# Optimization experiments

Measured on AMD Instinct MI355X. Metric: run time of the kernel, lower is better.

## Reference

```python
import jax, jax.numpy as jnp
import numpy as np

B, T, H, V = 4, 512, 2048, 32000
BETA = 0.1          # KL coefficient vs reference model
EPS_LOW = 0.2       # PPO clip lower
EPS_HIGH = 0.2      # PPO clip upper
TEMP = 1.0          # logit temperature


def _per_token_logps(h, w, ids):
    # h: [B,T,H], w: [V,H], ids: [B,T] -> log p(token_id) per position
    logits = jnp.einsum('bth,vh->btv', h, w) / TEMP          # [B,T,V]
    logps = jax.nn.log_softmax(logits.astype(jnp.float32), axis=-1)
    return jnp.take_along_axis(logps, ids[..., None], axis=-1)[..., 0]  # [B,T]


def setup_inputs() -> dict:
    key = jax.random.key(0)
    k = jax.random.split(key, 6)
    x = jax.random.normal(k[0], (B, T, H), jnp.float32)
    ref_input = jax.random.normal(k[1], (B, T, H), jnp.float32)
    lin_weight = jax.random.normal(k[2], (V, H), jnp.float32) * (H ** -0.5)
    ref_weight = jax.random.normal(k[3], (V, H), jnp.float32) * (H ** -0.5)
    selected_token_ids = jax.random.randint(k[4], (B, T), 0, V)
    attention_mask = jnp.ones((B, T), jnp.int32)
    advantages = jax.random.normal(k[5], (B,), jnp.float32)
    return {
        'x': x,
        'lin_weight': lin_weight,
        'ref_input': ref_input,
        'ref_weight': ref_weight,
        'advantages': advantages,
        'selected_token_ids': selected_token_ids,
        'attention_mask': attention_mask,
    }


def reference(x, lin_weight, ref_input, ref_weight, advantages,
              selected_token_ids, attention_mask):
    # policy per-token log-probs (fused linear + log-softmax + gather)
    logps = _per_token_logps(x, lin_weight, selected_token_ids)            # [B,T]
    # reference model path runs under no_grad in the original
    ref_logps = jax.lax.stop_gradient(
        _per_token_logps(ref_input, ref_weight, selected_token_ids))      # [B,T]
    # old_per_token_logps=None -> detached current logps (ratio==1 in fwd)
    old_logps = jax.lax.stop_gradient(logps)

    coef1 = jnp.exp(logps - old_logps)
    coef2 = jnp.clip(coef1, 1.0 - EPS_LOW, 1.0 + EPS_HIGH)
    adv = advantages[:, None]                                             # [B,1]
    per_token_loss = -jnp.minimum(coef1 * adv, coef2 * adv)

    # KL(ref || policy) surrogate: exp(d) - d - 1 with d = ref - cur
    d = ref_logps - logps
    kl = jnp.exp(d) - d - 1.0
    per_token_loss = per_token_loss + BETA * kl

    mask = attention_mask.astype(jnp.float32)
    # loss_type='bnpo': global masked token mean
    loss = jnp.sum(per_token_loss * mask) / jnp.maximum(jnp.sum(mask), 1.0)
    return loss
```

## Files before the change

### kernel.cpp

```cpp
#include <hip/hip_runtime.h>
#include <hip/hip_bf16.h>

#define B_ 4
#define T_ 512
#define H_ 2048
#define V_ 32000
#define M_ (B_ * T_)
#define BETA_ 0.1f

#define BM 128
#define BN 128
#define BK 32
#define NTILES (V_ / BN)
#define NP (NTILES * 2)
#define NPAD 512
#define GRID_LIN 4096

typedef __attribute__((ext_vector_type(8))) short short8;
typedef __attribute__((ext_vector_type(4))) float f32x4;

__device__ __forceinline__ void async_copy16(const void* g, void* l) {
  __builtin_amdgcn_global_load_lds(
      (const __attribute__((address_space(1))) void*)g,
      (__attribute__((address_space(3))) void*)l, 16, 0, 0);
}

__device__ __forceinline__ unsigned short f2bf(float f) {
  unsigned int u = __float_as_uint(f);
  u += 0x7fffu + ((u >> 16) & 1u);
  return (unsigned short)(u >> 16);
}

__global__ void cvt_bf16_kernel(const float* __restrict__ in,
                                unsigned short* __restrict__ out, int n4) {
  int i = blockIdx.x * blockDim.x + threadIdx.x;
  if (i < n4) {
    float4 v = ((const float4*)in)[i];
    ushort4 o;
    o.x = f2bf(v.x); o.y = f2bf(v.y); o.z = f2bf(v.z); o.w = f2bf(v.w);
    ((ushort4*)out)[i] = o;
  }
}

__global__ void sel_kernel(const float* __restrict__ x, const float* __restrict__ w,
                           const float* __restrict__ rx, const float* __restrict__ rw,
                           const int* __restrict__ ids, float* __restrict__ sel) {
  int gw = (blockIdx.x * 256 + threadIdx.x) >> 6;
  int l = threadIdx.x & 63;
  int md = gw >> 11;
  int m = gw & (M_ - 1);
  const float* xr = (md ? rx : x) + (size_t)m * H_;
  const float* wr = (md ? rw : w) + (size_t)ids[m] * H_;
  float s = 0.0f;
#pragma unroll
  for (int it = 0; it < H_ / 256; ++it) {
    int k = it * 256 + l * 4;
    float4 a = *(const float4*)(xr + k);
    float4 b = *(const float4*)(wr + k);
    s += a.x * b.x + a.y * b.y + a.z * b.z + a.w * b.w;
  }
#pragma unroll
  for (int off = 32; off; off >>= 1) s += __shfl_xor(s, off, 64);
  if (l == 0) sel[md * M_ + m] = s;
}

__global__ __launch_bounds__(256) void gemm_lse_kernel(
    const unsigned short* __restrict__ A,
    const unsigned short* __restrict__ Bw,
    float* __restrict__ pmax,
    float* __restrict__ psum) {
  const int linear = blockIdx.x;
  const int nt = (linear & 7) + 8 * (linear >> 7);
  if (nt >= NTILES) return;
  const int mb = (linear >> 3) & 15;

  __shared__ char smem[(BM + BN) * BK * 2];
  char* As = smem;
  char* Bs = smem + BM * BK * 2;

  const int tid = threadIdx.x;
  const int w = tid >> 6, l = tid & 63;
  const int quad = l >> 4, lr = l & 15;
  const int m0 = mb * BM, n0 = nt * BN;
  const int wm = (w >> 1) * 64, wn = (w & 1) * 64;

  const int s0 = tid, s1 = tid + 256;
  const unsigned short* gA0 = A + (size_t)(m0 + (s0 & 127)) * H_ + (s0 >> 7) * 8;
  const unsigned short* gA1 = A + (size_t)(m0 + (s1 & 127)) * H_ + (s1 >> 7) * 8;
  const unsigned short* gB0 = Bw + (size_t)(n0 + (s0 & 127)) * H_ + (s0 >> 7) * 8;
  const unsigned short* gB1 = Bw + (size_t)(n0 + (s1 & 127)) * H_ + (s1 >> 7) * 8;
  char* lA0 = As + s0 * 16; char* lA1 = As + s1 * 16;
  char* lB0 = Bs + s0 * 16; char* lB1 = Bs + s1 * 16;

  f32x4 acc[4][4] = {};

  const char* aRd[4]; const char* bRd[4];
#pragma unroll
  for (int i = 0; i < 4; ++i) {
    aRd[i] = As + (quad * 128 + wm + i * 16 + lr) * 16;
    bRd[i] = Bs + (quad * 128 + wn + i * 16 + lr) * 16;
  }

  for (int kt = 0; kt < H_ / BK; ++kt) {
    async_copy16(gA0, lA0); async_copy16(gA1, lA1);
    async_copy16(gB0, lB0); async_copy16(gB1, lB1);
    gA0 += BK; gA1 += BK; gB0 += BK; gB1 += BK;
    __syncthreads();
    short8 af[4], bf[4];
#pragma unroll
    for (int i = 0; i < 4; ++i) af[i] = *(const short8*)aRd[i];
#pragma unroll
    for (int j = 0; j < 4; ++j) bf[j] = *(const short8*)bRd[j];
#pragma unroll
    for (int i = 0; i < 4; ++i)
#pragma unroll
      for (int j = 0; j < 4; ++j)
        acc[i][j] = __builtin_amdgcn_mfma_f32_16x16x32_bf16(af[i], bf[j], acc[i][j], 0, 0, 0);
    __syncthreads();
  }

  const int p_idx = nt * 2 + (w & 1);
#pragma unroll
  for (int i = 0; i < 4; ++i) {
#pragma unroll
    for (int r = 0; r < 4; ++r) {
      float vmax = fmaxf(fmaxf(acc[i][0][r], acc[i][1][r]),
                         fmaxf(acc[i][2][r], acc[i][3][r]));
#pragma unroll
      for (int off = 8; off; off >>= 1) vmax = fmaxf(vmax, __shfl_xor(vmax, off, 64));
      float s = __expf(acc[i][0][r] - vmax) + __expf(acc[i][1][r] - vmax) +
                __expf(acc[i][2][r] - vmax) + __expf(acc[i][3][r] - vmax);
#pragma unroll
      for (int off = 8; off; off >>= 1) s += __shfl_xor(s, off, 64);
      if (lr == 0) {
        int mg = m0 + wm + i * 16 + quad * 4 + r;
        pmax[(size_t)mg * NPAD + p_idx] = vmax;
        psum[(size_t)mg * NPAD + p_idx] = s;
      }
    }
  }
}

__global__ void lse_merge_kernel(
    const float* __restrict__ pmaxP, const float* __restrict__ psumP,
    const float* __restrict__ pmaxR, const float* __restrict__ psumR,
    const float* __restrict__ sel, float* __restrict__ lp) {
  int gw = (blockIdx.x * 256 + threadIdx.x) >> 6;
  int l = threadIdx.x & 63;
  int md = gw >> 11, m = gw & (M_ - 1);
  const float* pm = (md ? pmaxR : pmaxP) + (size_t)m * NPAD;
  const float* ps = (md ? psumR : psumP) + (size_t)m * NPAD;
  float mx = -3.0e38f, s = 0.0f;
  for (int p = l; p < NP; p += 64) {
    float a = pm[p], b = ps[p];
    float nm = fmaxf(mx, a);
    s = s * __expf(mx - nm) + b * __expf(a - nm);
    mx = nm;
  }
#pragma unroll
  for (int off = 32; off; off >>= 1) {
    float omx = __shfl_xor(mx, off, 64);
    float os  = __shfl_xor(s, off, 64);
    float nm = fmaxf(mx, omx);
    s = s * __expf(mx - nm) + os * __expf(omx - nm);
    mx = nm;
  }
  if (l == 0) lp[md * M_ + m] = sel[md * M_ + m] - (mx + __logf(s));
}

__global__ void loss_kernel(const float* __restrict__ lp,
                            const float* __restrict__ adv,
                            const int* __restrict__ mask,
                            float* __restrict__ out) {
  __shared__ float sp[16], sm[16];
  int t = threadIdx.x;
  float pt = 0.0f, mk = 0.0f;
  for (int m = t; m < M_; m += 1024) {
    float d = lp[M_ + m] - lp[m];
    float kl = __expf(d) - d - 1.0f;
    float mkm = (float)mask[m];
    pt += (-adv[m >> 9] + BETA_ * kl) * mkm;
    mk += mkm;
  }
#pragma unroll
  for (int off = 32; off; off >>= 1) {
    pt += __shfl_xor(pt, off, 64);
    mk += __shfl_xor(mk, off, 64);
  }
  int wv = t >> 6, l = t & 63;
  if (l == 0) { sp[wv] = pt; sm[wv] = mk; }
  __syncthreads();
  if (t == 0) {
    float a = 0.0f, b = 0.0f;
#pragma unroll
    for (int i = 0; i < 16; ++i) { a += sp[i]; b += sm[i]; }
    out[0] = a / fmaxf(b, 1.0f);
  }
}

extern "C" void kernel_launch(void* const* d_in, const int* in_sizes, int n_in,
                              void* d_out, int out_size, void* d_ws, size_t ws_size,
                              hipStream_t stream) {
  const float* x    = (const float*)d_in[0];
  const float* lw   = (const float*)d_in[1];
  const float* rx   = (const float*)d_in[2];
  const float* rw   = (const float*)d_in[3];
  const float* adv  = (const float*)d_in[4];
  const int*   ids  = (const int*)d_in[5];
  const int*   mask = (const int*)d_in[6];
  float* out = (float*)d_out;

  char* ws = (char*)d_ws;
  unsigned short* Wb = (unsigned short*)ws;
  unsigned short* xb = (unsigned short*)(ws + (size_t)V_ * H_ * 2);
  char* p0 = ws + (size_t)V_ * H_ * 2 + (size_t)M_ * H_ * 2;
  const size_t PSZ = (size_t)M_ * NPAD * 4;
  float* pmaxP = (float*)(p0);
  float* psumP = (float*)(p0 + 1 * PSZ);
  float* pmaxR = (float*)(p0 + 2 * PSZ);
  float* psumR = (float*)(p0 + 3 * PSZ);
  float* sel   = (float*)(p0 + 4 * PSZ);
  float* lp    = (float*)(p0 + 4 * PSZ + 2 * M_ * 4);

  const int n4x = M_ * H_ / 4, n4w = V_ * H_ / 4;

  cvt_bf16_kernel<<<(n4x + 255) / 256, 256, 0, stream>>>(x, xb, n4x);
  cvt_bf16_kernel<<<(n4w + 255) / 256, 256, 0, stream>>>(lw, Wb, n4w);
  sel_kernel<<<(2 * M_) / 4, 256, 0, stream>>>(x, lw, rx, rw, ids, sel);
  gemm_lse_kernel<<<GRID_LIN, 256, 0, stream>>>(xb, Wb, pmaxP, psumP);
  cvt_bf16_kernel<<<(n4x + 255) / 256, 256, 0, stream>>>(rx, xb, n4x);
  cvt_bf16_kernel<<<(n4w + 255) / 256, 256, 0, stream>>>(rw, Wb, n4w);
  gemm_lse_kernel<<<GRID_LIN, 256, 0, stream>>>(xb, Wb, pmaxR, psumR);

  lse_merge_kernel<<<(2 * M_) / 4, 256, 0, stream>>>(pmaxP, psumP, pmaxR, psumR,
                                                     sel, lp);
  loss_kernel<<<1, 1024, 0, stream>>>(lp, adv, mask, out);
}
```

Before: 1.656 ms.

## Enlarge GEMM tiles to 256x256x64 with double-buffered LDS pipeline

The fused GEMM+LSE kernel moves from 128x128x32 tiles with 4 waves to 256x256x64 tiles with 8 waves. Each wave now computes a 128x64 sub-tile, and the LDS buffers are double-buffered so that global-to-LDS async loads of the next K slice overlap the MFMAs on the current one, with one barrier per iteration. s_setprio is raised around the MFMA bursts. The aim is more data reuse per loaded byte and fewer barrier stalls. The costs are 128 KB of dynamic LDS, higher register pressure from 32 accumulators per wave, and fewer blocks (125x8 tiles) to fill the CUs.

After: 1.689 ms. Within noise of the previous version (+2.0%).

```diff
diff --git a/kernel.cpp b/kernel.cpp
--- a/kernel.cpp
+++ b/kernel.cpp
@@ -8,13 +8,18 @@
 #define M_ (B_ * T_)
 #define BETA_ 0.1f
 
-#define BM 128
-#define BN 128
-#define BK 32
+#define BM 256
+#define BN 256
+#define BK 64
+#define NKT (H_ / BK)
 #define NTILES (V_ / BN)
-#define NP (NTILES * 2)
+#define NP (NTILES * 4)
 #define NPAD 512
-#define GRID_LIN 4096
+#define GRID_GEMM 1024
+
+#define ABYTES (BM * BK * 2)
+#define BUFBYTES (2 * ABYTES)
+#define LDS_TOTAL (2 * BUFBYTES)
 
 typedef __attribute__((ext_vector_type(8))) short short8;
 typedef __attribute__((ext_vector_type(4))) float f32x4;
@@ -64,64 +69,84 @@
   if (l == 0) sel[md * M_ + m] = s;
 }
 
-__global__ __launch_bounds__(256) void gemm_lse_kernel(
+__global__ __launch_bounds__(512, 2) void gemm_lse_kernel(
     const unsigned short* __restrict__ A,
     const unsigned short* __restrict__ Bw,
     float* __restrict__ pmax,
     float* __restrict__ psum) {
   const int linear = blockIdx.x;
-  const int nt = (linear & 7) + 8 * (linear >> 7);
+  const int c = linear & 7, g = linear >> 3;
+  const int nt = (g >> 3) * 8 + c;
   if (nt >= NTILES) return;
-  const int mb = (linear >> 3) & 15;
-
-  __shared__ char smem[(BM + BN) * BK * 2];
-  char* As = smem;
-  char* Bs = smem + BM * BK * 2;
+  const int mb = g & 7;
+
+  extern __shared__ char smem[];
 
   const int tid = threadIdx.x;
   const int w = tid >> 6, l = tid & 63;
   const int quad = l >> 4, lr = l & 15;
+  const int wr = w >> 2, wc = w & 3;
   const int m0 = mb * BM, n0 = nt * BN;
-  const int wm = (w >> 1) * 64, wn = (w & 1) * 64;
-
-  const int s0 = tid, s1 = tid + 256;
-  const unsigned short* gA0 = A + (size_t)(m0 + (s0 & 127)) * H_ + (s0 >> 7) * 8;
-  const unsigned short* gA1 = A + (size_t)(m0 + (s1 & 127)) * H_ + (s1 >> 7) * 8;
-  const unsigned short* gB0 = Bw + (size_t)(n0 + (s0 & 127)) * H_ + (s0 >> 7) * 8;
-  const unsigned short* gB1 = Bw + (size_t)(n0 + (s1 & 127)) * H_ + (s1 >> 7) * 8;
-  char* lA0 = As + s0 * 16; char* lA1 = As + s1 * 16;
-  char* lB0 = Bs + s0 * 16; char* lB1 = Bs + s1 * 16;
-
-  f32x4 acc[4][4] = {};
-
-  const char* aRd[4]; const char* bRd[4];
-#pragma unroll
-  for (int i = 0; i < 4; ++i) {
-    aRd[i] = As + (quad * 128 + wm + i * 16 + lr) * 16;
-    bRd[i] = Bs + (quad * 128 + wn + i * 16 + lr) * 16;
-  }
-
-  for (int kt = 0; kt < H_ / BK; ++kt) {
-    async_copy16(gA0, lA0); async_copy16(gA1, lA1);
-    async_copy16(gB0, lB0); async_copy16(gB1, lB1);
-    gA0 += BK; gA1 += BK; gB0 += BK; gB1 += BK;
+
+  const int srow = tid & 255, shi = tid >> 8;
+  const unsigned short* gA = A + (size_t)(m0 + srow) * H_ + shi * 8;
+  const unsigned short* gB = Bw + (size_t)(n0 + srow) * H_ + shi * 8;
+  const int ldsoff = (shi * 256 + srow) * 16;
+
+  f32x4 acc[8][4] = {};
+
+  const int abOff = quad * 4096 + (wr * 128 + lr) * 16;
+  const int bbOff = ABYTES + quad * 4096 + (wc * 64 + lr) * 16;
+
+  auto stage = [&](int p, int kt) {
+    const unsigned short* a = gA + kt * BK;
+    const unsigned short* b = gB + kt * BK;
+    char* la = smem + p * BUFBYTES + ldsoff;
+    char* lb = la + ABYTES;
+#pragma unroll
+    for (int j = 0; j < 4; ++j) {
+      async_copy16(a + j * 16, la + j * 8192);
+      async_copy16(b + j * 16, lb + j * 8192);
+    }
+  };
+
+  auto compute = [&](int p) {
+    const char* ab = smem + p * BUFBYTES + abOff;
+    const char* bb = smem + p * BUFBYTES + bbOff;
+#pragma unroll
+    for (int kk = 0; kk < 2; ++kk) {
+      short8 af[8], bf[4];
+#pragma unroll
+      for (int i = 0; i < 8; ++i)
+        af[i] = *(const short8*)(ab + kk * 16384 + i * 256);
+#pragma unroll
+      for (int j = 0; j < 4; ++j)
+        bf[j] = *(const short8*)(bb + kk * 16384 + j * 256);
+      __builtin_amdgcn_s_setprio(1);
+#pragma unroll
+      for (int i = 0; i < 8; ++i)
+#pragma unroll
+        for (int j = 0; j < 4; ++j)
+          acc[i][j] = __builtin_amdgcn_mfma_f32_16x16x32_bf16(
+              af[i], bf[j], acc[i][j], 0, 0, 0);
+      __builtin_amdgcn_s_setprio(0);
+    }
+  };
+
+  stage(0, 0);
+  __syncthreads();
+  int p = 0;
+  for (int kt = 1; kt < NKT; ++kt) {
+    stage(p ^ 1, kt);
+    compute(p);
     __syncthreads();
-    short8 af[4], bf[4];
-#pragma unroll
-    for (int i = 0; i < 4; ++i) af[i] = *(const short8*)aRd[i];
-#pragma unroll
-    for (int j = 0; j < 4; ++j) bf[j] = *(const short8*)bRd[j];
-#pragma unroll
-    for (int i = 0; i < 4; ++i)
-#pragma unroll
-      for (int j = 0; j < 4; ++j)
-        acc[i][j] = __builtin_amdgcn_mfma_f32_16x16x32_bf16(af[i], bf[j], acc[i][j], 0, 0, 0);
-    __syncthreads();
-  }
-
-  const int p_idx = nt * 2 + (w & 1);
-#pragma unroll
-  for (int i = 0; i < 4; ++i) {
+    p ^= 1;
+  }
+  compute(p);
+
+  const int p_idx = nt * 4 + wc;
+#pragma unroll
+  for (int i = 0; i < 8; ++i) {
 #pragma unroll
     for (int r = 0; r < 4; ++r) {
       float vmax = fmaxf(fmaxf(acc[i][0][r], acc[i][1][r]),
@@ -133,7 +158,7 @@
 #pragma unroll
       for (int off = 8; off; off >>= 1) s += __shfl_xor(s, off, 64);
       if (lr == 0) {
-        int mg = m0 + wm + i * 16 + quad * 4 + r;
+        int mg = m0 + wr * 128 + i * 16 + quad * 4 + r;
         pmax[(size_t)mg * NPAD + p_idx] = vmax;
         psum[(size_t)mg * NPAD + p_idx] = s;
       }
@@ -210,6 +235,13 @@
   const int*   mask = (const int*)d_in[6];
   float* out = (float*)d_out;
 
+  static bool s_attr_set = false;
+  if (!s_attr_set) {
+    hipFuncSetAttribute(reinterpret_cast<const void*>(gemm_lse_kernel),
+                        hipFuncAttributeMaxDynamicSharedMemorySize, LDS_TOTAL);
+    s_attr_set = true;
+  }
+
   char* ws = (char*)d_ws;
   unsigned short* Wb = (unsigned short*)ws;
   unsigned short* xb = (unsigned short*)(ws + (size_t)V_ * H_ * 2);
@@ -227,10 +259,10 @@
   cvt_bf16_kernel<<<(n4x + 255) / 256, 256, 0, stream>>>(x, xb, n4x);
   cvt_bf16_kernel<<<(n4w + 255) / 256, 256, 0, stream>>>(lw, Wb, n4w);
   sel_kernel<<<(2 * M_) / 4, 256, 0, stream>>>(x, lw, rx, rw, ids, sel);
-  gemm_lse_kernel<<<GRID_LIN, 256, 0, stream>>>(xb, Wb, pmaxP, psumP);
+  gemm_lse_kernel<<<GRID_GEMM, 512, LDS_TOTAL, stream>>>(xb, Wb, pmaxP, psumP);
   cvt_bf16_kernel<<<(n4x + 255) / 256, 256, 0, stream>>>(rx, xb, n4x);
   cvt_bf16_kernel<<<(n4w + 255) / 256, 256, 0, stream>>>(rw, Wb, n4w);
-  gemm_lse_kernel<<<GRID_LIN, 256, 0, stream>>>(xb, Wb, pmaxR, psumR);
+  gemm_lse_kernel<<<GRID_GEMM, 512, LDS_TOTAL, stream>>>(xb, Wb, pmaxR, psumR);
 
   lse_merge_kernel<<<(2 * M_) / 4, 256, 0, stream>>>(pmaxP, psumP, pmaxR, psumR,
                                                      sel, lp);
```
